# Performance work log

Measured on AMD Instinct MI355X. Metric: run time of the kernel, lower is better.

## Reference

```python
import jax, jax.numpy as jnp
import numpy as np

K = 25        # moving_avg_window
PAD = (K - 1) // 2
EPS = 1e-8


def _decompose(x):
    # x: [B, S, C]
    B, S, C = x.shape
    # --- trend: AvgPool1d(kernel=K, stride=1, padding=PAD), count_include_pad=True
    # zero-pad then windowed sum, always divide by K (matches torch default).
    sums = jax.lax.reduce_window(
        x, jnp.float32(0.0).astype(x.dtype), jax.lax.add,
        window_dimensions=(1, K, 1), window_strides=(1, 1, 1),
        padding=((0, 0), (PAD, PAD), (0, 0)))
    trend = sums / K  # [B, S, C]

    # --- initial seasonal: FFT along time, zero out first half of bins
    # (including DC), take real part of inverse FFT.
    half = S // 2
    freq_mask = (jnp.arange(S) >= half)[None, :, None]  # [1, S, 1]
    dft = jnp.fft.fft(x, axis=1)
    seasonal0 = jnp.fft.ifft(dft * freq_mask, axis=1).real.astype(x.dtype)

    # --- degrees of trend/seasonality per (batch, channel)
    # Reference uses the robust fallback residual = x - trend - seasonal0
    # (the STL path in the original is a per-series scipy call; its fallback
    # defines the same math).
    resid = x - trend - seasonal0
    var = lambda v: jnp.var(v, axis=1, ddof=1)  # torch.var is unbiased -> ddof=1; [B, C]
    var_res = var(resid)
    d_t = jnp.clip(1.0 - var_res / (var(trend + resid) + EPS), 0.0, 1.0)
    d_s = jnp.clip(1.0 - var_res / (var(seasonal0 + resid) + EPS), 0.0, 1.0)

    # --- final seasonal: multiplicative if strong trend/seasonality, else additive
    cond = ((d_t > 0.5) | (d_s > 0.5))[:, None, :]  # [B, 1, C]
    seasonal = jnp.where(cond, x / (trend + EPS), x - trend)
    return trend, seasonal


def setup_inputs() -> dict:
    key = jax.random.key(0)
    x = jax.random.normal(key, (32, 4096, 128), dtype=jnp.float32)
    return {"x": x}


def reference(x):
    return _decompose(x)
```

## Files before the change

### kernel.cpp

```cpp
#include <hip/hip_runtime.h>

#define SS 4096
#define CC 128
#define BB 32
#define KW 25
#define PADW 12
#define CH 64
#define SROWS (CH + KW - 1)
#define CPB 8
#define NSERIES (BB * CC)
#define STAGE_F4 (SROWS * CC / 4)

typedef float f4v __attribute__((ext_vector_type(4)));
typedef float f2v __attribute__((ext_vector_type(2)));

__global__ __launch_bounds__(512)
void kb_pass(const float* __restrict__ x, float* __restrict__ trend,
             float* __restrict__ seasonal, float* __restrict__ stats) {
    __shared__ f4v stage[2][STAGE_F4];
    __shared__ f2v sred[7][7][64];

    const int blk = blockIdx.x;
    const int b = blk >> 3;
    const int q = blk & 7;
    const int tid = threadIdx.x;
    const int cp = tid & 63;
    const int rg = tid >> 6;
    const float* __restrict__ xb = x + (size_t)b * SS * CC;
    f2v* __restrict__ tb = (f2v*)(trend + (size_t)b * SS * CC);
    f2v* __restrict__ sv = (f2v*)(seasonal + (size_t)b * SS * CC);

    {
        const int sbase = q * (CPB * CH) - PADW;
        f4v v0[6];
        #pragma unroll
        for (int t = 0; t < 6; ++t) {
            const int idx = t * 512 + tid;
            if (idx < STAGE_F4) {
                const int srow = sbase + (idx >> 5);
                const int crow = srow < 0 ? 0 : (srow >= SS ? SS - 1 : srow);
                v0[t] = *(const f4v*)(xb + (size_t)crow * CC + ((idx & 31) << 2));
            }
        }
        #pragma unroll
        for (int t = 0; t < 6; ++t) {
            const int idx = t * 512 + tid;
            if (idx < STAGE_F4) {
                f4v w = v0[t];
                const int srow = sbase + (idx >> 5);
                if (srow < 0 || srow >= SS) w = (f4v){0.f, 0.f, 0.f, 0.f};
                stage[0][idx] = w;
            }
        }
    }

    f4v vals[4];
    auto issue = [&](int c) {
        const int sbase = q * (CPB * CH) + c * CH - PADW;
        #pragma unroll
        for (int t = 0; t < 4; ++t) {
            const int nidx = t * 512 + tid;
            const int srow = sbase + 24 + (nidx >> 5);
            const int crow = srow >= SS ? SS - 1 : srow;
            vals[t] = *(const f4v*)(xb + (size_t)crow * CC + ((nidx & 31) << 2));
        }
    };
    auto commit = [&](int c, int buf) {
        const f2v* src = (const f2v*)stage[buf ^ 1];
        f2v* dst = (f2v*)stage[buf];
        #pragma unroll
        for (int t = 0; t < 3; ++t) {
            const int hidx = t * 512 + tid;
            dst[hidx] = src[64 * 64 + hidx];
        }
        const int sbase = q * (CPB * CH) + c * CH - PADW;
        #pragma unroll
        for (int t = 0; t < 4; ++t) {
            const int nidx = t * 512 + tid;
            const int srow = sbase + 24 + (nidx >> 5);
            f4v w = vals[t];
            if (srow >= SS) w = (f4v){0.f, 0.f, 0.f, 0.f};
            stage[buf][768 + nidx] = w;
        }
    };

    f2v Sx_e = {0,0}, Sx_o = {0,0}, Sx2 = {0,0};
    f2v St_e = {0,0}, St_o = {0,0}, St2 = {0,0}, Sxt = {0,0};

    for (int c = 0; c < CPB; ++c) {
        __syncthreads();
        const int cur = c & 1;
        if (c + 1 < CPB) issue(c + 1);

        const int S0 = q * (CPB * CH) + c * CH;
        const int r0 = rg * 8;
        const f2v* stg = (const f2v*)stage[cur];

        f2v win[KW];
        #pragma unroll
        for (int j = 0; j < KW; ++j) win[j] = stg[(r0 + j) * 64 + cp];

        #pragma unroll
        for (int i = 0; i < 8; ++i) {
            float ax = win[0].x, ay = win[0].y;
            #pragma unroll
            for (int j = 1; j < KW; ++j) { ax += win[j].x; ay += win[j].y; }
            f2v tf;
            tf.x = ax / 25.0f;
            tf.y = ay / 25.0f;
            const int row = (S0 + r0 + i) * 64 + cp;
            __builtin_nontemporal_store(tf, &tb[row]);

            const f2v xv = win[PADW];
            f2v so;
            so.x = xv.x / (tf.x + 1e-8f);
            so.y = xv.y / (tf.y + 1e-8f);
            __builtin_nontemporal_store(so, &sv[row]);

            if (i & 1) { Sx_o.x += xv.x; Sx_o.y += xv.y; St_o.x += tf.x; St_o.y += tf.y; }
            else       { Sx_e.x += xv.x; Sx_e.y += xv.y; St_e.x += tf.x; St_e.y += tf.y; }
            Sx2.x += xv.x * xv.x;  Sx2.y += xv.y * xv.y;
            St2.x += tf.x * tf.x;  St2.y += tf.y * tf.y;
            Sxt.x += xv.x * tf.x;  Sxt.y += xv.y * tf.y;

            #pragma unroll
            for (int j = 0; j < KW - 1; ++j) win[j] = win[j + 1];
            if (i < 7) win[KW - 1] = stg[(r0 + i + KW) * 64 + cp];
        }

        if (c + 1 < CPB) commit(c + 1, cur ^ 1);
    }

    if (rg > 0) {
        f2v* me = &sred[rg - 1][0][cp];
        me[0*64] = Sx_e; me[1*64] = Sx_o; me[2*64] = Sx2;
        me[3*64] = St_e; me[4*64] = St_o; me[5*64] = St2;
        me[6*64] = Sxt;
    }
    __syncthreads();
    if (rg == 0) {
        #pragma unroll
        for (int g = 0; g < 7; ++g) {
            const f2v* gp = &sred[g][0][cp];
            Sx_e.x += gp[0*64].x; Sx_e.y += gp[0*64].y;
            Sx_o.x += gp[1*64].x; Sx_o.y += gp[1*64].y;
            Sx2.x  += gp[2*64].x; Sx2.y  += gp[2*64].y;
            St_e.x += gp[3*64].x; St_e.y += gp[3*64].y;
            St_o.x += gp[4*64].x; St_o.y += gp[4*64].y;
            St2.x  += gp[5*64].x; St2.y  += gp[5*64].y;
            Sxt.x  += gp[6*64].x; Sxt.y  += gp[6*64].y;
        }
        const int series = b * CC + 2 * cp;
        float* sp = stats + (size_t)q * NSERIES + series;
        const size_t jstride = (size_t)CPB * NSERIES;
        *(f2v*)(sp + 0 * jstride) = Sx_e;
        *(f2v*)(sp + 1 * jstride) = Sx_o;
        *(f2v*)(sp + 2 * jstride) = Sx2;
        *(f2v*)(sp + 3 * jstride) = St_e;
        *(f2v*)(sp + 4 * jstride) = St_o;
        *(f2v*)(sp + 5 * jstride) = St2;
        *(f2v*)(sp + 6 * jstride) = Sxt;
    }
}

__global__ __launch_bounds__(256)
void k2_finalize_fix(const float* __restrict__ stats, const float* __restrict__ x,
                     const float* __restrict__ trend, float* __restrict__ seasonal) {
    const int j = threadIdx.x >> 5;
    const int sl = threadIdx.x & 31;
    const int series0 = blockIdx.x * 32;
    const size_t jstride = (size_t)CPB * NSERIES;

    __shared__ float red[32][8];
    __shared__ int nf;
    __shared__ int flist[32];
    if (threadIdx.x == 0) nf = 0;
    if (j < 7) {
        const float* p = stats + j * jstride + series0 + sl;
        float a = 0.f;
        #pragma unroll
        for (int k = 0; k < CPB; ++k) a += p[(size_t)k * NSERIES];
        red[sl][j] = a;
    }
    __syncthreads();
    if (threadIdx.x < 32) {
        const int me = threadIdx.x;
        const float Sx_e = red[me][0], Sx_o = red[me][1], Sx2 = red[me][2];
        const float St_e = red[me][3], St_o = red[me][4], St2 = red[me][5];
        const float Sxt = red[me][6];

        const float Sf = (float)SS;
        const float halfS = 0.5f * Sf;
        const float c_e = Sx_o / Sf;
        const float c_o = Sx_e / Sf;
        const float sum_c = halfS * (c_e + c_o);
        const float sumsq_c = halfS * (c_e * c_e + c_o * c_o);

        const float Sw_e = 0.5f * Sx_e - St_e;
        const float Sw_o = 0.5f * Sx_o - St_o;
        const float Sw2 = 0.25f * Sx2 - Sxt + St2;

        const float s1 = (Sw_e + Sw_o) + sum_c;
        const float q1 = Sw2 + 2.f * (c_e * Sw_e + c_o * Sw_o) + sumsq_c;
        const float var1 = (q1 - s1 * s1 / Sf) / (Sf - 1.f);
        const float s2 = 0.5f * (Sx_e + Sx_o) + sum_c;
        const float q2 = 0.25f * Sx2 + (c_e * Sx_e + c_o * Sx_o) + sumsq_c;
        const float var2 = (q2 - s2 * s2 / Sf) / (Sf - 1.f);
        const float Sa = (Sx_e + Sx_o) - (St_e + St_o);
        const float Sa2 = Sx2 - 2.f * Sxt + St2;
        const float var3 = (Sa2 - Sa * Sa / Sf) / (Sf - 1.f);

        const float d_t = 1.f - var1 / (var2 + 1e-8f);
        const float d_s = 1.f - var1 / (var3 + 1e-8f);
        if (!(d_t > 0.5f || d_s > 0.5f)) {
            const int i = atomicAdd(&nf, 1);
            flist[i] = series0 + me;
        }
    }
    __syncthreads();
    for (int fi = 0; fi < nf; ++fi) {
        const int sr = flist[fi];
        const int b = sr >> 7, ch = sr & 127;
        const float* xs = x + (size_t)b * SS * CC + ch;
        const float* ts = trend + (size_t)b * SS * CC + ch;
        float* so = seasonal + (size_t)b * SS * CC + ch;
        for (int s = threadIdx.x; s < SS; s += 256)
            so[(size_t)s * CC] = xs[(size_t)s * CC] - ts[(size_t)s * CC];
    }
}

extern "C" void kernel_launch(void* const* d_in, const int* in_sizes, int n_in,
                              void* d_out, int out_size, void* d_ws, size_t ws_size,
                              hipStream_t stream) {
    const float* x = (const float*)d_in[0];
    float* out = (float*)d_out;
    float* trend = out;
    float* seasonal = out + (size_t)BB * SS * CC;

    float* stats = (float*)d_ws;

    kb_pass<<<dim3(BB * 8), dim3(512), 0, stream>>>(x, trend, seasonal, stats);
    k2_finalize_fix<<<dim3(NSERIES / 32), dim3(256), 0, stream>>>(stats, x, trend, seasonal);
}
```

Baseline: 40.64 us.

## Fuse finalize into main pass via last-block ticket and halve chunk size

Merges the second kernel into the main pass. The last block to finish each batch, detected with an atomic ticket counter, reduces the per-strip statistics and rewrites any additive-path series. Chunk height drops from 64 to 32 rows, so there are twice as many blocks (16 strips per batch). The reduction scratch now reuses the staging LDS, and launch bounds request 4 blocks per CU. Nontemporal stores are replaced by ordinary stores. This removes a kernel launch and improves occupancy and parallelism, at the cost of a memset, threadfences and more halo re-reads.

```diff
diff --git a/kernel.cpp b/kernel.cpp
--- a/kernel.cpp
+++ b/kernel.cpp
@@ -5,24 +5,30 @@
 #define BB 32
 #define KW 25
 #define PADW 12
-#define CH 64
+#define CH 32
 #define SROWS (CH + KW - 1)
 #define CPB 8
+#define ROWSPB (CH * CPB)
+#define NSTRIP (SS / ROWSPB)
 #define NSERIES (BB * CC)
 #define STAGE_F4 (SROWS * CC / 4)
 
 typedef float f4v __attribute__((ext_vector_type(4)));
 typedef float f2v __attribute__((ext_vector_type(2)));
 
-__global__ __launch_bounds__(512)
+__global__ __launch_bounds__(512, 4)
 void kb_pass(const float* __restrict__ x, float* __restrict__ trend,
-             float* __restrict__ seasonal, float* __restrict__ stats) {
+             float* __restrict__ seasonal, float* __restrict__ stats,
+             int* __restrict__ cnt) {
     __shared__ f4v stage[2][STAGE_F4];
-    __shared__ f2v sred[7][7][64];
+    __shared__ float fin[7][128];
+    __shared__ int ticket_s, nf;
+    __shared__ int flist[128];
 
     const int blk = blockIdx.x;
-    const int b = blk >> 3;
-    const int q = blk & 7;
+    const int b = blk >> 4;
+    const int st = blk & 15;
+    const int s0 = st * ROWSPB;
     const int tid = threadIdx.x;
     const int cp = tid & 63;
     const int rg = tid >> 6;
@@ -31,34 +37,25 @@
     f2v* __restrict__ sv = (f2v*)(seasonal + (size_t)b * SS * CC);
 
     {
-        const int sbase = q * (CPB * CH) - PADW;
-        f4v v0[6];
-        #pragma unroll
-        for (int t = 0; t < 6; ++t) {
+        const int sbase = s0 - PADW;
+        #pragma unroll
+        for (int t = 0; t < 4; ++t) {
             const int idx = t * 512 + tid;
             if (idx < STAGE_F4) {
                 const int srow = sbase + (idx >> 5);
                 const int crow = srow < 0 ? 0 : (srow >= SS ? SS - 1 : srow);
-                v0[t] = *(const f4v*)(xb + (size_t)crow * CC + ((idx & 31) << 2));
+                f4v v = *(const f4v*)(xb + (size_t)crow * CC + ((idx & 31) << 2));
+                if (srow < 0 || srow >= SS) v = (f4v){0.f, 0.f, 0.f, 0.f};
+                stage[0][idx] = v;
             }
         }
-        #pragma unroll
-        for (int t = 0; t < 6; ++t) {
-            const int idx = t * 512 + tid;
-            if (idx < STAGE_F4) {
-                f4v w = v0[t];
-                const int srow = sbase + (idx >> 5);
-                if (srow < 0 || srow >= SS) w = (f4v){0.f, 0.f, 0.f, 0.f};
-                stage[0][idx] = w;
-            }
-        }
-    }
-
-    f4v vals[4];
+    }
+
+    f4v vals[2];
     auto issue = [&](int c) {
-        const int sbase = q * (CPB * CH) + c * CH - PADW;
-        #pragma unroll
-        for (int t = 0; t < 4; ++t) {
+        const int sbase = s0 + c * CH - PADW;
+        #pragma unroll
+        for (int t = 0; t < 2; ++t) {
             const int nidx = t * 512 + tid;
             const int srow = sbase + 24 + (nidx >> 5);
             const int crow = srow >= SS ? SS - 1 : srow;
@@ -71,11 +68,11 @@
         #pragma unroll
         for (int t = 0; t < 3; ++t) {
             const int hidx = t * 512 + tid;
-            dst[hidx] = src[64 * 64 + hidx];
-        }
-        const int sbase = q * (CPB * CH) + c * CH - PADW;
-        #pragma unroll
-        for (int t = 0; t < 4; ++t) {
+            dst[hidx] = src[CH * 64 + hidx];
+        }
+        const int sbase = s0 + c * CH - PADW;
+        #pragma unroll
+        for (int t = 0; t < 2; ++t) {
             const int nidx = t * 512 + tid;
             const int srow = sbase + 24 + (nidx >> 5);
             f4v w = vals[t];
@@ -92,8 +89,8 @@
         const int cur = c & 1;
         if (c + 1 < CPB) issue(c + 1);
 
-        const int S0 = q * (CPB * CH) + c * CH;
-        const int r0 = rg * 8;
+        const int Rb = s0 + c * CH;
+        const int r0 = rg * 4;
         const f2v* stg = (const f2v*)stage[cur];
 
         f2v win[KW];
@@ -101,21 +98,21 @@
         for (int j = 0; j < KW; ++j) win[j] = stg[(r0 + j) * 64 + cp];
 
         #pragma unroll
-        for (int i = 0; i < 8; ++i) {
+        for (int i = 0; i < 4; ++i) {
             float ax = win[0].x, ay = win[0].y;
             #pragma unroll
             for (int j = 1; j < KW; ++j) { ax += win[j].x; ay += win[j].y; }
             f2v tf;
             tf.x = ax / 25.0f;
             tf.y = ay / 25.0f;
-            const int row = (S0 + r0 + i) * 64 + cp;
-            __builtin_nontemporal_store(tf, &tb[row]);
+            const int row = (Rb + r0 + i) * 64 + cp;
+            tb[row] = tf;
 
             const f2v xv = win[PADW];
             f2v so;
             so.x = xv.x / (tf.x + 1e-8f);
             so.y = xv.y / (tf.y + 1e-8f);
-            __builtin_nontemporal_store(so, &sv[row]);
+            sv[row] = so;
 
             if (i & 1) { Sx_o.x += xv.x; Sx_o.y += xv.y; St_o.x += tf.x; St_o.y += tf.y; }
             else       { Sx_e.x += xv.x; Sx_e.y += xv.y; St_e.x += tf.x; St_e.y += tf.y; }
@@ -125,14 +122,16 @@
 
             #pragma unroll
             for (int j = 0; j < KW - 1; ++j) win[j] = win[j + 1];
-            if (i < 7) win[KW - 1] = stg[(r0 + i + KW) * 64 + cp];
+            if (i < 3) win[KW - 1] = stg[(r0 + i + KW) * 64 + cp];
         }
 
         if (c + 1 < CPB) commit(c + 1, cur ^ 1);
     }
 
+    __syncthreads();
+    f2v* sr = (f2v*)stage;
     if (rg > 0) {
-        f2v* me = &sred[rg - 1][0][cp];
+        f2v* me = sr + (size_t)(rg - 1) * 7 * 64 + cp;
         me[0*64] = Sx_e; me[1*64] = Sx_o; me[2*64] = Sx2;
         me[3*64] = St_e; me[4*64] = St_o; me[5*64] = St2;
         me[6*64] = Sxt;
@@ -141,7 +140,7 @@
     if (rg == 0) {
         #pragma unroll
         for (int g = 0; g < 7; ++g) {
-            const f2v* gp = &sred[g][0][cp];
+            const f2v* gp = sr + (size_t)g * 7 * 64 + cp;
             Sx_e.x += gp[0*64].x; Sx_e.y += gp[0*64].y;
             Sx_o.x += gp[1*64].x; Sx_o.y += gp[1*64].y;
             Sx2.x  += gp[2*64].x; Sx2.y  += gp[2*64].y;
@@ -151,8 +150,8 @@
             Sxt.x  += gp[6*64].x; Sxt.y  += gp[6*64].y;
         }
         const int series = b * CC + 2 * cp;
-        float* sp = stats + (size_t)q * NSERIES + series;
-        const size_t jstride = (size_t)CPB * NSERIES;
+        float* sp = stats + (size_t)st * NSERIES + series;
+        const size_t jstride = (size_t)NSTRIP * NSERIES;
         *(f2v*)(sp + 0 * jstride) = Sx_e;
         *(f2v*)(sp + 1 * jstride) = Sx_o;
         *(f2v*)(sp + 2 * jstride) = Sx2;
@@ -161,70 +160,68 @@
         *(f2v*)(sp + 5 * jstride) = St2;
         *(f2v*)(sp + 6 * jstride) = Sxt;
     }
-}
-
-__global__ __launch_bounds__(256)
-void k2_finalize_fix(const float* __restrict__ stats, const float* __restrict__ x,
-                     const float* __restrict__ trend, float* __restrict__ seasonal) {
-    const int j = threadIdx.x >> 5;
-    const int sl = threadIdx.x & 31;
-    const int series0 = blockIdx.x * 32;
-    const size_t jstride = (size_t)CPB * NSERIES;
-
-    __shared__ float red[32][8];
-    __shared__ int nf;
-    __shared__ int flist[32];
-    if (threadIdx.x == 0) nf = 0;
-    if (j < 7) {
-        const float* p = stats + j * jstride + series0 + sl;
-        float a = 0.f;
-        #pragma unroll
-        for (int k = 0; k < CPB; ++k) a += p[(size_t)k * NSERIES];
-        red[sl][j] = a;
-    }
-    __syncthreads();
-    if (threadIdx.x < 32) {
-        const int me = threadIdx.x;
-        const float Sx_e = red[me][0], Sx_o = red[me][1], Sx2 = red[me][2];
-        const float St_e = red[me][3], St_o = red[me][4], St2 = red[me][5];
-        const float Sxt = red[me][6];
+
+    __syncthreads();
+    if (tid == 0) {
+        __threadfence();
+        ticket_s = atomicAdd(&cnt[b], 1);
+    }
+    __syncthreads();
+    if (ticket_s != NSTRIP - 1) return;
+
+    __threadfence();
+    if (tid < 448) {
+        const int j = tid >> 6, c2 = tid & 63;
+        const float* p = stats + (size_t)j * NSTRIP * NSERIES + b * CC + 2 * c2;
+        f2v a = {0.f, 0.f};
+        #pragma unroll
+        for (int k = 0; k < NSTRIP; ++k) {
+            const f2v v = *(const f2v*)(p + (size_t)k * NSERIES);
+            a.x += v.x; a.y += v.y;
+        }
+        fin[j][2 * c2] = a.x; fin[j][2 * c2 + 1] = a.y;
+    }
+    if (tid == 0) nf = 0;
+    __syncthreads();
+    if (tid < 128) {
+        const int ch = tid;
+        const float Sx_eF = fin[0][ch], Sx_oF = fin[1][ch], Sx2F = fin[2][ch];
+        const float St_eF = fin[3][ch], St_oF = fin[4][ch], St2F = fin[5][ch];
+        const float SxtF = fin[6][ch];
 
         const float Sf = (float)SS;
         const float halfS = 0.5f * Sf;
-        const float c_e = Sx_o / Sf;
-        const float c_o = Sx_e / Sf;
+        const float c_e = Sx_oF / Sf;
+        const float c_o = Sx_eF / Sf;
         const float sum_c = halfS * (c_e + c_o);
         const float sumsq_c = halfS * (c_e * c_e + c_o * c_o);
 
-        const float Sw_e = 0.5f * Sx_e - St_e;
-        const float Sw_o = 0.5f * Sx_o - St_o;
-        const float Sw2 = 0.25f * Sx2 - Sxt + St2;
+        const float Sw_e = 0.5f * Sx_eF - St_eF;
+        const float Sw_o = 0.5f * Sx_oF - St_oF;
+        const float Sw2 = 0.25f * Sx2F - SxtF + St2F;
 
         const float s1 = (Sw_e + Sw_o) + sum_c;
         const float q1 = Sw2 + 2.f * (c_e * Sw_e + c_o * Sw_o) + sumsq_c;
         const float var1 = (q1 - s1 * s1 / Sf) / (Sf - 1.f);
-        const float s2 = 0.5f * (Sx_e + Sx_o) + sum_c;
-        const float q2 = 0.25f * Sx2 + (c_e * Sx_e + c_o * Sx_o) + sumsq_c;
+        const float s2 = 0.5f * (Sx_eF + Sx_oF) + sum_c;
+        const float q2 = 0.25f * Sx2F + (c_e * Sx_eF + c_o * Sx_oF) + sumsq_c;
         const float var2 = (q2 - s2 * s2 / Sf) / (Sf - 1.f);
-        const float Sa = (Sx_e + Sx_o) - (St_e + St_o);
-        const float Sa2 = Sx2 - 2.f * Sxt + St2;
+        const float Sa = (Sx_eF + Sx_oF) - (St_eF + St_oF);
+        const float Sa2 = Sx2F - 2.f * SxtF + St2F;
         const float var3 = (Sa2 - Sa * Sa / Sf) / (Sf - 1.f);
 
         const float d_t = 1.f - var1 / (var2 + 1e-8f);
         const float d_s = 1.f - var1 / (var3 + 1e-8f);
-        if (!(d_t > 0.5f || d_s > 0.5f)) {
-            const int i = atomicAdd(&nf, 1);
-            flist[i] = series0 + me;
-        }
+        if (!(d_t > 0.5f || d_s > 0.5f))
+            flist[atomicAdd(&nf, 1)] = ch;
     }
     __syncthreads();
     for (int fi = 0; fi < nf; ++fi) {
-        const int sr = flist[fi];
-        const int b = sr >> 7, ch = sr & 127;
+        const int ch = flist[fi];
         const float* xs = x + (size_t)b * SS * CC + ch;
         const float* ts = trend + (size_t)b * SS * CC + ch;
         float* so = seasonal + (size_t)b * SS * CC + ch;
-        for (int s = threadIdx.x; s < SS; s += 256)
+        for (int s = tid; s < SS; s += 512)
             so[(size_t)s * CC] = xs[(size_t)s * CC] - ts[(size_t)s * CC];
     }
 }
@@ -238,7 +235,9 @@
     float* seasonal = out + (size_t)BB * SS * CC;
 
     float* stats = (float*)d_ws;
-
-    kb_pass<<<dim3(BB * 8), dim3(512), 0, stream>>>(x, trend, seasonal, stats);
-    k2_finalize_fix<<<dim3(NSERIES / 32), dim3(256), 0, stream>>>(stats, x, trend, seasonal);
+    int* cnt = (int*)(stats + 7 * NSTRIP * NSERIES);
+
+    hipMemsetAsync(cnt, 0, BB * sizeof(int), stream);
+    kb_pass<<<dim3(BB * NSTRIP), dim3(512), 0, stream>>>(x, trend, seasonal,
+                                                         stats, cnt);
 }
```

New measurement: 96.53 us. +137.5%, slower.

## Split channel dimension across two blocks to double grid size

Applied to the files above, without the earlier changes.

Each block now handles half of the 128 channels (64) for its time segment, so the grid grows from 256 to 512 blocks. Each thread covers 4 rows per chunk instead of 8, the LDS staging buffer is halved, and the stats reduction reuses the staging buffer in place of a separate array. The goal is better occupancy and coverage of the GPU's compute units. In exchange, the 24-row window halo is loaded and copied relative to less work per block, and row reads are narrower (256 bytes per row).

```diff
diff --git a/kernel.cpp b/kernel.cpp
--- a/kernel.cpp
+++ b/kernel.cpp
@@ -8,8 +8,10 @@
 #define CH 64
 #define SROWS (CH + KW - 1)
 #define CPB 8
+#define HC 64
+#define HCP 32
 #define NSERIES (BB * CC)
-#define STAGE_F4 (SROWS * CC / 4)
+#define STAGE_F4 (SROWS * HC / 4)
 
 typedef float f4v __attribute__((ext_vector_type(4)));
 typedef float f2v __attribute__((ext_vector_type(2)));
@@ -18,69 +20,61 @@
 void kb_pass(const float* __restrict__ x, float* __restrict__ trend,
              float* __restrict__ seasonal, float* __restrict__ stats) {
     __shared__ f4v stage[2][STAGE_F4];
-    __shared__ f2v sred[7][7][64];
 
     const int blk = blockIdx.x;
-    const int b = blk >> 3;
-    const int q = blk & 7;
+    const int b = blk >> 4;
+    const int q = (blk >> 1) & 7;
+    const int h = blk & 1;
     const int tid = threadIdx.x;
-    const int cp = tid & 63;
-    const int rg = tid >> 6;
-    const float* __restrict__ xb = x + (size_t)b * SS * CC;
-    f2v* __restrict__ tb = (f2v*)(trend + (size_t)b * SS * CC);
-    f2v* __restrict__ sv = (f2v*)(seasonal + (size_t)b * SS * CC);
+    const int cp = tid & 31;
+    const int rg = tid >> 5;
+    const float* __restrict__ xbh = x + (size_t)b * SS * CC + h * HC;
+    f2v* __restrict__ tb2 = (f2v*)(trend + (size_t)b * SS * CC);
+    f2v* __restrict__ sv2 = (f2v*)(seasonal + (size_t)b * SS * CC);
+    const int co = h * HCP + 0;
 
     {
         const int sbase = q * (CPB * CH) - PADW;
-        f4v v0[6];
-        #pragma unroll
-        for (int t = 0; t < 6; ++t) {
+        #pragma unroll
+        for (int t = 0; t < 3; ++t) {
             const int idx = t * 512 + tid;
             if (idx < STAGE_F4) {
-                const int srow = sbase + (idx >> 5);
+                const int srow = sbase + (idx >> 4);
                 const int crow = srow < 0 ? 0 : (srow >= SS ? SS - 1 : srow);
-                v0[t] = *(const f4v*)(xb + (size_t)crow * CC + ((idx & 31) << 2));
+                f4v v = *(const f4v*)(xbh + (size_t)crow * CC + ((idx & 15) << 2));
+                if (srow < 0 || srow >= SS) v = (f4v){0.f, 0.f, 0.f, 0.f};
+                stage[0][idx] = v;
             }
         }
-        #pragma unroll
-        for (int t = 0; t < 6; ++t) {
-            const int idx = t * 512 + tid;
-            if (idx < STAGE_F4) {
-                f4v w = v0[t];
-                const int srow = sbase + (idx >> 5);
-                if (srow < 0 || srow >= SS) w = (f4v){0.f, 0.f, 0.f, 0.f};
-                stage[0][idx] = w;
-            }
-        }
-    }
-
-    f4v vals[4];
+    }
+
+    f4v vals[2];
     auto issue = [&](int c) {
         const int sbase = q * (CPB * CH) + c * CH - PADW;
         #pragma unroll
-        for (int t = 0; t < 4; ++t) {
+        for (int t = 0; t < 2; ++t) {
             const int nidx = t * 512 + tid;
-            const int srow = sbase + 24 + (nidx >> 5);
+            const int srow = sbase + 24 + (nidx >> 4);
             const int crow = srow >= SS ? SS - 1 : srow;
-            vals[t] = *(const f4v*)(xb + (size_t)crow * CC + ((nidx & 31) << 2));
+            vals[t] = *(const f4v*)(xbh + (size_t)crow * CC + ((nidx & 15) << 2));
         }
     };
     auto commit = [&](int c, int buf) {
         const f2v* src = (const f2v*)stage[buf ^ 1];
         f2v* dst = (f2v*)stage[buf];
         #pragma unroll
-        for (int t = 0; t < 3; ++t) {
+        for (int t = 0; t < 2; ++t) {
             const int hidx = t * 512 + tid;
-            dst[hidx] = src[64 * 64 + hidx];
+            if (hidx < 24 * HCP) dst[hidx] = src[CH * HCP + hidx];
         }
         const int sbase = q * (CPB * CH) + c * CH - PADW;
         #pragma unroll
-        for (int t = 0; t < 4; ++t) {
+        for (int t = 0; t < 2; ++t) {
             const int nidx = t * 512 + tid;
-            const int srow = sbase + 24 + (nidx >> 5);
+            const int srow = sbase + 24 + (nidx >> 4);
             f4v w = vals[t];
             if (srow >= SS) w = (f4v){0.f, 0.f, 0.f, 0.f};
-            stage[buf][768 + nidx] = w;
+            stage[buf][384 + nidx] = w;
         }
     };
 
@@ -93,29 +87,29 @@
         if (c + 1 < CPB) issue(c + 1);
 
         const int S0 = q * (CPB * CH) + c * CH;
-        const int r0 = rg * 8;
+        const int r0 = rg * 4;
         const f2v* stg = (const f2v*)stage[cur];
 
         f2v win[KW];
         #pragma unroll
-        for (int j = 0; j < KW; ++j) win[j] = stg[(r0 + j) * 64 + cp];
-
-        #pragma unroll
-        for (int i = 0; i < 8; ++i) {
+        for (int j = 0; j < KW; ++j) win[j] = stg[(r0 + j) * HCP + cp];
+
+        #pragma unroll
+        for (int i = 0; i < 4; ++i) {
             float ax = win[0].x, ay = win[0].y;
             #pragma unroll
             for (int j = 1; j < KW; ++j) { ax += win[j].x; ay += win[j].y; }
             f2v tf;
             tf.x = ax / 25.0f;
             tf.y = ay / 25.0f;
-            const int row = (S0 + r0 + i) * 64 + cp;
-            __builtin_nontemporal_store(tf, &tb[row]);
+            const int row = (S0 + r0 + i) * 64 + co + cp;
+            __builtin_nontemporal_store(tf, &tb2[row]);
 
             const f2v xv = win[PADW];
             f2v so;
             so.x = xv.x / (tf.x + 1e-8f);
             so.y = xv.y / (tf.y + 1e-8f);
-            __builtin_nontemporal_store(so, &sv[row]);
+            __builtin_nontemporal_store(so, &sv2[row]);
 
             if (i & 1) { Sx_o.x += xv.x; Sx_o.y += xv.y; St_o.x += tf.x; St_o.y += tf.y; }
             else       { Sx_e.x += xv.x; Sx_e.y += xv.y; St_e.x += tf.x; St_e.y += tf.y; }
@@ -125,32 +119,34 @@
 
             #pragma unroll
             for (int j = 0; j < KW - 1; ++j) win[j] = win[j + 1];
-            if (i < 7) win[KW - 1] = stg[(r0 + i + KW) * 64 + cp];
+            if (i < 3) win[KW - 1] = stg[(r0 + i + KW) * HCP + cp];
         }
 
         if (c + 1 < CPB) commit(c + 1, cur ^ 1);
     }
 
+    __syncthreads();
+    f2v* sr = (f2v*)stage;
     if (rg > 0) {
-        f2v* me = &sred[rg - 1][0][cp];
-        me[0*64] = Sx_e; me[1*64] = Sx_o; me[2*64] = Sx2;
-        me[3*64] = St_e; me[4*64] = St_o; me[5*64] = St2;
-        me[6*64] = Sxt;
+        f2v* me = sr + (size_t)(rg - 1) * 7 * HCP + cp;
+        me[0*HCP] = Sx_e; me[1*HCP] = Sx_o; me[2*HCP] = Sx2;
+        me[3*HCP] = St_e; me[4*HCP] = St_o; me[5*HCP] = St2;
+        me[6*HCP] = Sxt;
     }
     __syncthreads();
     if (rg == 0) {
         #pragma unroll
-        for (int g = 0; g < 7; ++g) {
-            const f2v* gp = &sred[g][0][cp];
-            Sx_e.x += gp[0*64].x; Sx_e.y += gp[0*64].y;
-            Sx_o.x += gp[1*64].x; Sx_o.y += gp[1*64].y;
-            Sx2.x  += gp[2*64].x; Sx2.y  += gp[2*64].y;
-            St_e.x += gp[3*64].x; St_e.y += gp[3*64].y;
-            St_o.x += gp[4*64].x; St_o.y += gp[4*64].y;
-            St2.x  += gp[5*64].x; St2.y  += gp[5*64].y;
-            Sxt.x  += gp[6*64].x; Sxt.y  += gp[6*64].y;
-        }
-        const int series = b * CC + 2 * cp;
+        for (int g = 0; g < 15; ++g) {
+            const f2v* gp = sr + (size_t)g * 7 * HCP + cp;
+            Sx_e.x += gp[0*HCP].x; Sx_e.y += gp[0*HCP].y;
+            Sx_o.x += gp[1*HCP].x; Sx_o.y += gp[1*HCP].y;
+            Sx2.x  += gp[2*HCP].x; Sx2.y  += gp[2*HCP].y;
+            St_e.x += gp[3*HCP].x; St_e.y += gp[3*HCP].y;
+            St_o.x += gp[4*HCP].x; St_o.y += gp[4*HCP].y;
+            St2.x  += gp[5*HCP].x; St2.y  += gp[5*HCP].y;
+            Sxt.x  += gp[6*HCP].x; Sxt.y  += gp[6*HCP].y;
+        }
+        const int series = b * CC + h * HC + 2 * cp;
         float* sp = stats + (size_t)q * NSERIES + series;
         const size_t jstride = (size_t)CPB * NSERIES;
         *(f2v*)(sp + 0 * jstride) = Sx_e;
@@ -239,6 +235,6 @@
 
     float* stats = (float*)d_ws;
 
-    kb_pass<<<dim3(BB * 8), dim3(512), 0, stream>>>(x, trend, seasonal, stats);
+    kb_pass<<<dim3(BB * 16), dim3(512), 0, stream>>>(x, trend, seasonal, stats);
     k2_finalize_fix<<<dim3(NSERIES / 32), dim3(256), 0, stream>>>(stats, x, trend, seasonal);
 }
```

After: 39.85 us. No clear change (-1.9%).
